# Kernel optimization log

Hardware: AMD Instinct MI355X
Metric: run time of the kernel (lower is better)

The kernel has to match this reference:

```python
import jax, jax.numpy as jnp
import numpy as np

DIM = 64
N_HOP = 2
N_MEM = 32
BATCH = 512
N_ENT = 200000
N_REL = 32
KGE_W = 0.01
L2_W = 1e-7
EPS = 1e-7  # BCE clamp for stability


def setup_inputs() -> dict:
    key = jax.random.key(0)
    ks = jax.random.split(key, 11)
    return {
        "items": jax.random.randint(ks[0], (BATCH,), 0, N_ENT),
        "labels": jax.random.randint(ks[1], (BATCH,), 0, 2),
        "memories_h": jax.random.randint(ks[2], (N_HOP, BATCH, N_MEM), 0, N_ENT),
        "memories_r": jax.random.randint(ks[3], (N_HOP, BATCH, N_MEM), 0, N_REL),
        "memories_t": jax.random.randint(ks[4], (N_HOP, BATCH, N_MEM), 0, N_ENT),
        "entity_emb": jax.random.normal(ks[5], (N_ENT, DIM), jnp.float32) * 0.1,
        "relation_emb": jax.random.normal(ks[6], (N_REL, DIM * DIM), jnp.float32) * 0.02,
        "gru_wih": jax.random.normal(ks[7], (3 * DIM, DIM), jnp.float32) * 0.1,
        "gru_whh": jax.random.normal(ks[8], (3 * DIM, DIM), jnp.float32) * 0.1,
        "gru_bih": jnp.zeros((3 * DIM,), jnp.float32),
        "gru_bhh": jnp.zeros((3 * DIM,), jnp.float32),
    }


def _gru_scan(x_seq, h0, wih, whh, bih, bhh):
    """PyTorch nn.GRU on a 2D input treats dim 0 as the sequence axis (unbatched).
    x_seq: [B, D] scanned over B; h0: [D]. Gate order: r, z, n."""
    def step(h, x):
        gi = wih @ x + bih          # [3D]
        gh = whh @ h + bhh          # [3D]
        ir, iz, inn = jnp.split(gi, 3)
        hr, hz, hn = jnp.split(gh, 3)
        r = jax.nn.sigmoid(ir + hr)
        z = jax.nn.sigmoid(iz + hz)
        n = jnp.tanh(inn + r * hn)
        h_new = (1.0 - z) * n + z * h
        return h_new, h_new
    h_final, ys = jax.lax.scan(step, h0, x_seq)
    return ys, h_final


def reference(items, labels, memories_h, memories_r, memories_t,
              entity_emb, relation_emb, gru_wih, gru_whh, gru_bih, gru_bhh):
    item_emb = entity_emb[items]                                # [B, D]
    h_emb = entity_emb[memories_h]                              # [H, B, M, D]
    t_emb = entity_emb[memories_t]                              # [H, B, M, D]
    r_flat = relation_emb[memories_r]                           # [H, B, M, D*D]
    r_emb = r_flat.reshape(N_HOP, BATCH, N_MEM, DIM, DIM)       # [H, B, M, D, D]

    h_state = jnp.zeros((DIM,), item_emb.dtype)
    o_sum = jnp.zeros_like(item_emb)
    for hop in range(N_HOP):
        Rh = jnp.einsum('bmij,bmj->bmi', r_emb[hop], h_emb[hop])   # [B, M, D]
        probs = jax.nn.softmax(jnp.einsum('bmi,bi->bm', Rh, item_emb), axis=1)
        o = jnp.einsum('bm,bmd->bd', probs, t_emb[hop])            # [B, D]
        # GRU recurrence over the batch axis (faithful to the 2D-input quirk)
        item_emb, h_state = _gru_scan(item_emb, h_state, gru_wih, gru_whh, gru_bih, gru_bhh)
        o_sum = o_sum + o  # using_all_hops=True -> sum of all hops

    scores = jax.nn.sigmoid(jnp.sum(item_emb * o_sum, axis=1))     # [B]

    # losses
    lbl = labels.astype(scores.dtype)
    s = jnp.clip(scores, EPS, 1.0 - EPS)
    base_loss = -jnp.mean(lbl * jnp.log(s) + (1.0 - lbl) * jnp.log1p(-s))

    hRt = jnp.einsum('hbmi,hbmij,hbmj->hbm', h_emb, r_emb, t_emb)  # [H, B, M]
    kge_loss = -KGE_W * jnp.sum(jnp.mean(jax.nn.sigmoid(hRt), axis=(1, 2)))

    l2_loss = L2_W * (jnp.sum(h_emb * h_emb) + jnp.sum(t_emb * t_emb) + jnp.sum(r_flat * r_flat))

    loss = base_loss + kge_loss + l2_loss
    return scores, base_loss, kge_loss, l2_loss, loss
```

## Files before the change

kernel.cpp:

```cpp
#include <hip/hip_runtime.h>

#define DIM   64
#define G3    192
#define NB    512
#define NM    32
#define NRELS 32
#define CH    32
#define NCH   (NB/CH)
#define KGE_W 0.01f
#define L2_W  1e-7f
#define EPSC  1e-7f


__device__ inline float bcast(float v, int srclane) {
    return __int_as_float(__builtin_amdgcn_readlane(__float_as_int(v), srclane));
}

__device__ inline float sigmoidf_(float x) { return 1.0f / (1.0f + __expf(-x)); }
__device__ inline float tanhf_(float x)    { return 1.0f - 2.0f / (1.0f + __expf(2.0f * x)); }

__device__ inline float wave_sum(float v) {
#pragma unroll
    for (int off = 32; off > 0; off >>= 1) v += __shfl_xor(v, off, 64);
    return v;
}
__device__ inline float wave_max(float v) {
#pragma unroll
    for (int off = 32; off > 0; off >>= 1) v = fmaxf(v, __shfl_xor(v, off, 64));
    return v;
}


#define FOR32(F) F(0)F(1)F(2)F(3)F(4)F(5)F(6)F(7)F(8)F(9)F(10)F(11)F(12)F(13)F(14)F(15) \
                 F(16)F(17)F(18)F(19)F(20)F(21)F(22)F(23)F(24)F(25)F(26)F(27)F(28)F(29)F(30)F(31)
#define FOR16A(F) F(0)F(1)F(2)F(3)F(4)F(5)F(6)F(7)F(8)F(9)F(10)F(11)F(12)F(13)F(14)F(15)
#define FOR16B(F) F(16)F(17)F(18)F(19)F(20)F(21)F(22)F(23)F(24)F(25)F(26)F(27)F(28)F(29)F(30)F(31)

#define F16U(x) ((unsigned)__builtin_bit_cast(unsigned short, (_Float16)(x)))


__device__ __forceinline__ void gru_scan_staged(float (*gibuf)[CH * G3],
                                                const float* __restrict__ GI,
                                                const float* __restrict__ whh,
                                                const float* __restrict__ bhh,
                                                const float* __restrict__ h0,
                                                float* __restrict__ ys,
                                                float* __restrict__ hfin_out)
{
    const int tid  = threadIdx.x;
    const int lane = tid & 63;
    const int wave = tid >> 6;

    if (wave != 0) {
        const int sid = tid - 64;
        const float4* src = (const float4*)GI;
        float4* dst = (float4*)gibuf[0];
#pragma unroll
        for (int j = 0; j < 8; ++j) dst[sid + j * 192] = src[sid + j * 192];
    }
    __syncthreads();

    if (wave == 0) {
        const float* wrp = whh + (0 * DIM + lane) * DIM;
        const float* wzp = whh + (1 * DIM + lane) * DIM;
        const float* wnp = whh + (2 * DIM + lane) * DIM;

#define DWP(j) unsigned uwr##j, uwz##j, uwn##j;
        FOR32(DWP)
#undef DWP
#define LWP(j) uwr##j = F16U(wrp[(j)]) | (F16U(wrp[(j)+32]) << 16); \
               uwz##j = F16U(wzp[(j)]) | (F16U(wzp[(j)+32]) << 16); \
               uwn##j = F16U(wnp[(j)]) | (F16U(wnp[(j)+32]) << 16);
        FOR32(LWP)
#undef LWP

        const float br = bhh[lane], bz = bhh[DIM + lane], bn = bhh[2 * DIM + lane];
        float h = h0 ? h0[lane] : 0.0f;

        for (int c = 0; c < NCH; ++c) {
            const float* buf = gibuf[c & 1];
            for (int tl = 0; tl < CH; ++tl) {
                const float* gi = buf + tl * G3;
                float c0 = gi[lane], c1 = gi[DIM + lane], c2 = gi[2 * DIM + lane];

                float A = h, B = h;
                asm("v_permlane32_swap_b32 %0, %1" : "+v"(A), "+v"(B));
                unsigned packed = __builtin_bit_cast(unsigned,
                                     __builtin_amdgcn_cvt_pkrtz(A, B));

#define RL(j) unsigned hp##j = (unsigned)__builtin_amdgcn_readlane((int)packed, j);
                FOR32(RL)
#undef RL

                float ar0 = br, ar1 = 0.f, az0 = bz, az1 = 0.f, an0 = bn, an1 = 0.f;
#define SJ0(j) { asm("v_dot2_f32_f16 %0, %1, %2, %0" : "+v"(ar0) : "v"(uwr##j), "s"(hp##j)); \
                 asm("v_dot2_f32_f16 %0, %1, %2, %0" : "+v"(az0) : "v"(uwz##j), "s"(hp##j)); \
                 asm("v_dot2_f32_f16 %0, %1, %2, %0" : "+v"(an0) : "v"(uwn##j), "s"(hp##j)); }
                FOR16A(SJ0)
#undef SJ0
#define SJ1(j) { asm("v_dot2_f32_f16 %0, %1, %2, %0" : "+v"(ar1) : "v"(uwr##j), "s"(hp##j)); \
                 asm("v_dot2_f32_f16 %0, %1, %2, %0" : "+v"(az1) : "v"(uwz##j), "s"(hp##j)); \
                 asm("v_dot2_f32_f16 %0, %1, %2, %0" : "+v"(an1) : "v"(uwn##j), "s"(hp##j)); }
                FOR16B(SJ1)
#undef SJ1

                float ghr = ar0 + ar1;
                float ghz = az0 + az1;
                float ghn = an0 + an1;

                float r = sigmoidf_(c0 + ghr);
                float z = sigmoidf_(c1 + ghz);
                float n = tanhf_(c2 + r * ghn);
                h = n + z * (h - n);

                ys[(c * CH + tl) * DIM + lane] = h;
            }
            __syncthreads();
        }
        if (hfin_out) hfin_out[lane] = h;
    } else {
        const int sid = tid - 64;
        for (int c = 0; c < NCH; ++c) {
            if (c + 1 < NCH) {
                const float4* src = (const float4*)(GI + (size_t)(c + 1) * CH * G3);
                float4* dst = (float4*)gibuf[(c + 1) & 1];
#pragma unroll
                for (int j = 0; j < 8; ++j) dst[sid + j * 192] = src[sid + j * 192];
            }
            __syncthreads();
        }
    }
}


__global__ __launch_bounds__(64) void gi_kernel(const float* __restrict__ xsrc,
                                                const int* __restrict__ idx,
                                                const float* __restrict__ wih,
                                                const float* __restrict__ bih,
                                                const float* __restrict__ Rel,
                                                float* __restrict__ GI,
                                                float* __restrict__ relnorm)
{
    const int blk = blockIdx.x, lane = threadIdx.x;
    if (blk >= NB) {
        const int r = blk - NB;
        const float* R = Rel + r * DIM * DIM;
        float a = 0.0f;
#pragma unroll 4
        for (int i = 0; i < DIM; ++i) { float v = R[i * DIM + lane]; a = fmaf(v, v, a); }
        a = wave_sum(a);
        if (lane == 0) relnorm[r] = a;
        return;
    }
    const int b = blk;
    float xv = idx ? xsrc[idx[b] * DIM + lane] : xsrc[b * DIM + lane];
    float a0 = bih[lane], a1 = bih[DIM + lane], a2 = bih[2 * DIM + lane];
    const float* w0 = wih + (0 * DIM + lane) * DIM;
    const float* w1 = wih + (1 * DIM + lane) * DIM;
    const float* w2 = wih + (2 * DIM + lane) * DIM;
#pragma unroll 4
    for (int k = 0; k < DIM; ++k) {
        float xk = bcast(xv, k);
        a0 = fmaf(w0[k], xk, a0);
        a1 = fmaf(w1[k], xk, a1);
        a2 = fmaf(w2[k], xk, a2);
    }
    float* gp = GI + b * G3;
    gp[lane] = a0; gp[DIM + lane] = a1; gp[2 * DIM + lane] = a2;
}


__global__ __launch_bounds__(256, 1) void fused0(const float* __restrict__ E,
                                              const float* __restrict__ Rel,
                                              const int* __restrict__ items,
                                              const int* __restrict__ mh,
                                              const int* __restrict__ mr,
                                              const int* __restrict__ mt,
                                              const float* __restrict__ GI,
                                              const float* __restrict__ whh,
                                              const float* __restrict__ bhh,
                                              const float* __restrict__ relnorm,
                                              float* __restrict__ ys0,
                                              float* __restrict__ hfin,
                                              float* __restrict__ o0,
                                              float* __restrict__ kge_part,
                                              float* __restrict__ l2_part)
{
    __shared__ __align__(16) float gibuf[2][CH * G3];
    __shared__ float logits[NM], probs[NM], opart[4][DIM], wred[4][4];

    if (blockIdx.x == 0) {
        gru_scan_staged(gibuf, GI, whh, bhh, nullptr, ys0, hfin);
        return;
    }

    const int b = blockIdx.x - 1;
    const int tid = threadIdx.x, lane = tid & 63, wave = tid >> 6;

    float iv = E[items[b] * DIM + lane];
    float kge0 = 0.0f, kge1 = 0.0f, l2acc = 0.0f, r2acc = 0.0f;

    for (int mm = 0; mm < 8; ++mm) {
        const int m = wave * 8 + mm;
        const int base = b * NM + m;
        const int hidx = mh[base], ridx = mr[base], tidx = mt[base];
        float hv = E[hidx * DIM + lane];
        float tv = E[tidx * DIM + lane];
        l2acc = fmaf(hv, hv, l2acc);
        l2acc = fmaf(tv, tv, l2acc);
        r2acc += relnorm[ridx];
        const float* R = Rel + ridx * DIM * DIM;
        float accA = 0.0f, accK = 0.0f;
#pragma unroll 4
        for (int i = 0; i < DIM; ++i) {
            float rv = R[i * DIM + lane];
            accA = fmaf(bcast(iv, i), rv, accA);
            accK = fmaf(bcast(hv, i), rv, accK);
        }
        float la = wave_sum(accA * hv);
        float lk = wave_sum(accK * tv);
        if (lane == 0) logits[m] = la;
        kge0 += sigmoidf_(lk);
    }
    for (int mm = 0; mm < 8; ++mm) {
        const int m = wave * 8 + mm;
        const int base = NB * NM + b * NM + m;
        const int hidx = mh[base], ridx = mr[base], tidx = mt[base];
        float hv = E[hidx * DIM + lane];
        float tv = E[tidx * DIM + lane];
        l2acc = fmaf(hv, hv, l2acc);
        l2acc = fmaf(tv, tv, l2acc);
        r2acc += relnorm[ridx];
        const float* R = Rel + ridx * DIM * DIM;
        float accK = 0.0f;
#pragma unroll 4
        for (int i = 0; i < DIM; ++i)
            accK = fmaf(bcast(hv, i), R[i * DIM + lane], accK);
        kge1 += sigmoidf_(wave_sum(accK * tv));
    }
    __syncthreads();

    if (wave == 0) {
        float v = (lane < NM) ? logits[lane] : -1e30f;
        float mx = wave_max(v);
        float e = (lane < NM) ? __expf(v - mx) : 0.0f;
        float ssum = wave_sum(e);
        if (lane < NM) probs[lane] = e / ssum;
    }
    __syncthreads();

    float od = 0.0f;
    for (int mm = 0; mm < 8; ++mm) {
        const int m = wave * 8 + mm;
        const int tidx = mt[b * NM + m];
        od = fmaf(probs[m], E[tidx * DIM + lane], od);
    }
    opart[wave][lane] = od;
    float l2tot = wave_sum(l2acc);
    if (lane == 0) { wred[wave][0] = kge0; wred[wave][1] = kge1; wred[wave][2] = l2tot + r2acc; }
    __syncthreads();
    if (wave == 0)
        o0[b * DIM + lane] = opart[0][lane] + opart[1][lane] + opart[2][lane] + opart[3][lane];
    if (tid == 0) {
        kge_part[b * 2 + 0] = wred[0][0] + wred[1][0] + wred[2][0] + wred[3][0];
        kge_part[b * 2 + 1] = wred[0][1] + wred[1][1] + wred[2][1] + wred[3][1];
        l2_part[b]          = wred[0][2] + wred[1][2] + wred[2][2] + wred[3][2];
    }
}


__global__ __launch_bounds__(256, 1) void fused1(const float* __restrict__ E,
                                              const float* __restrict__ Rel,
                                              const int* __restrict__ mh,
                                              const int* __restrict__ mr,
                                              const int* __restrict__ mt,
                                              const float* __restrict__ GI,
                                              const float* __restrict__ whh,
                                              const float* __restrict__ bhh,
                                              const float* __restrict__ hfin,
                                              const float* __restrict__ ys0,
                                              float* __restrict__ ys1,
                                              const float* __restrict__ o0,
                                              float* __restrict__ osum)
{
    __shared__ __align__(16) float gibuf[2][CH * G3];
    __shared__ float logits[NM], probs[NM], opart[4][DIM];

    if (blockIdx.x == 0) {
        gru_scan_staged(gibuf, GI, whh, bhh, hfin, ys1, nullptr);
        return;
    }

    const int b = blockIdx.x - 1;
    const int tid = threadIdx.x, lane = tid & 63, wave = tid >> 6;

    float iv = ys0[b * DIM + lane];

    for (int mm = 0; mm < 8; ++mm) {
        const int m = wave * 8 + mm;
        const int base = NB * NM + b * NM + m;
        const int hidx = mh[base], ridx = mr[base];
        float hv = E[hidx * DIM + lane];
        const float* R = Rel + ridx * DIM * DIM;
        float accA = 0.0f;
#pragma unroll 4
        for (int i = 0; i < DIM; ++i)
            accA = fmaf(bcast(iv, i), R[i * DIM + lane], accA);
        float la = wave_sum(accA * hv);
        if (lane == 0) logits[m] = la;
    }
    __syncthreads();
    if (wave == 0) {
        float v = (lane < NM) ? logits[lane] : -1e30f;
        float mx = wave_max(v);
        float e = (lane < NM) ? __expf(v - mx) : 0.0f;
        float ssum = wave_sum(e);
        if (lane < NM) probs[lane] = e / ssum;
    }
    __syncthreads();
    float od = 0.0f;
    for (int mm = 0; mm < 8; ++mm) {
        const int m = wave * 8 + mm;
        const int tidx = mt[NB * NM + b * NM + m];
        od = fmaf(probs[m], E[tidx * DIM + lane], od);
    }
    opart[wave][lane] = od;
    __syncthreads();
    if (wave == 0)
        osum[b * DIM + lane] = o0[b * DIM + lane] +
            opart[0][lane] + opart[1][lane] + opart[2][lane] + opart[3][lane];
}


__global__ __launch_bounds__(512) void finalize(const float* __restrict__ ys1,
                                                const float* __restrict__ osum,
                                                const int* __restrict__ labels,
                                                const float* __restrict__ kge_part,
                                                const float* __restrict__ l2_part,
                                                float* __restrict__ out)
{
    __shared__ float red[512];
    const int tid = threadIdx.x;

    float dot = 0.0f;
    const float* a = ys1 + tid * DIM;
    const float* c = osum + tid * DIM;
#pragma unroll 8
    for (int k = 0; k < DIM; ++k) dot = fmaf(a[k], c[k], dot);
    float score = sigmoidf_(dot);
    out[tid] = score;

    float s = fminf(fmaxf(score, EPSC), 1.0f - EPSC);
    float term = labels[tid] ? logf(s) : log1pf(-s);

    float bsum, ksum, lsum;
    {
        red[tid] = term; __syncthreads();
#pragma unroll
        for (int st = 256; st > 0; st >>= 1) { if (tid < st) red[tid] += red[tid + st]; __syncthreads(); }
        bsum = red[0]; __syncthreads();
    }
    {
        red[tid] = kge_part[2 * tid] + kge_part[2 * tid + 1]; __syncthreads();
#pragma unroll
        for (int st = 256; st > 0; st >>= 1) { if (tid < st) red[tid] += red[tid + st]; __syncthreads(); }
        ksum = red[0]; __syncthreads();
    }
    {
        red[tid] = l2_part[tid]; __syncthreads();
#pragma unroll
        for (int st = 256; st > 0; st >>= 1) { if (tid < st) red[tid] += red[tid + st]; __syncthreads(); }
        lsum = red[0];
    }

    if (tid == 0) {
        float base = -bsum / (float)NB;
        float kge  = -KGE_W * ksum / (float)(NB * NM);
        float l2   = L2_W * lsum;
        out[NB + 0] = base;
        out[NB + 1] = kge;
        out[NB + 2] = l2;
        out[NB + 3] = base + kge + l2;
    }
}


extern "C" void kernel_launch(void* const* d_in, const int* in_sizes, int n_in,
                              void* d_out, int out_size, void* d_ws, size_t ws_size,
                              hipStream_t stream) {
    const int*   items  = (const int*)d_in[0];
    const int*   labels = (const int*)d_in[1];
    const int*   mh     = (const int*)d_in[2];
    const int*   mr     = (const int*)d_in[3];
    const int*   mt     = (const int*)d_in[4];
    const float* E      = (const float*)d_in[5];
    const float* Rel    = (const float*)d_in[6];
    const float* wih    = (const float*)d_in[7];
    const float* whh    = (const float*)d_in[8];
    const float* bih    = (const float*)d_in[9];
    const float* bhh    = (const float*)d_in[10];
    float* out = (float*)d_out;
    float* ws  = (float*)d_ws;

    float* GI0     = ws;
    float* GI1     = GI0 + 98304;
    float* ys0     = GI1 + 98304;
    float* ys1     = ys0 + 32768;
    float* hfin    = ys1 + 32768;
    float* o0      = hfin + 64;
    float* osum    = o0 + 32768;
    float* relnorm = osum + 32768;
    float* kge_p   = relnorm + 32;
    float* l2_p    = kge_p + 1024;

    gi_kernel<<<NB + NRELS, 64, 0, stream>>>(E, items, wih, bih, Rel, GI0, relnorm);
    fused0<<<NB + 1, 256, 0, stream>>>(E, Rel, items, mh, mr, mt, GI0, whh, bhh,
                                       relnorm, ys0, hfin, o0, kge_p, l2_p);
    gi_kernel<<<NB, 64, 0, stream>>>(ys0, nullptr, wih, bih, Rel, GI1, relnorm);
    fused1<<<NB + 1, 256, 0, stream>>>(E, Rel, mh, mr, mt, GI1, whh, bhh, hfin,
                                       ys0, ys1, o0, osum);
    finalize<<<1, 512, 0, stream>>>(ys1, osum, labels, kge_p, l2_p, out);
}
```

Before: 452.4 us.

## Fuse hop-1 GRU input projection into hop-0 scan block and split dot chains

The second gi_kernel launch is removed. The helper waves in the GRU scan block now compute the hop-1 input projection (wih·ys0 + bih) in fp16 dot2, one chunk behind the sequential recurrence, and write it to GI1. The recurrence itself splits each gate's dot-product chain into four accumulators and computes r,z before n, to shorten dependency latency. Risks: fp16 rounding on the wih projection, and extra register pressure and work on the helper waves that share the serial scan's CU.

```diff
diff --git a/kernel.cpp b/kernel.cpp
--- a/kernel.cpp
+++ b/kernel.cpp
@@ -33,10 +33,31 @@
 
 #define FOR32(F) F(0)F(1)F(2)F(3)F(4)F(5)F(6)F(7)F(8)F(9)F(10)F(11)F(12)F(13)F(14)F(15) \
                  F(16)F(17)F(18)F(19)F(20)F(21)F(22)F(23)F(24)F(25)F(26)F(27)F(28)F(29)F(30)F(31)
-#define FOR16A(F) F(0)F(1)F(2)F(3)F(4)F(5)F(6)F(7)F(8)F(9)F(10)F(11)F(12)F(13)F(14)F(15)
-#define FOR16B(F) F(16)F(17)F(18)F(19)F(20)F(21)F(22)F(23)F(24)F(25)F(26)F(27)F(28)F(29)F(30)F(31)
+#define FOR8_0(F) F(0)F(1)F(2)F(3)F(4)F(5)F(6)F(7)
+#define FOR8_1(F) F(8)F(9)F(10)F(11)F(12)F(13)F(14)F(15)
+#define FOR8_2(F) F(16)F(17)F(18)F(19)F(20)F(21)F(22)F(23)
+#define FOR8_3(F) F(24)F(25)F(26)F(27)F(28)F(29)F(30)F(31)
 
 #define F16U(x) ((unsigned)__builtin_bit_cast(unsigned short, (_Float16)(x)))
+
+#define DOT(acc, w, s) asm("v_dot2_f32_f16 %0, %1, %2, %0" : "+v"(acc) : "v"(w), "s"(s));
+
+#define DW(j)  unsigned uwr##j, uwz##j, uwn##j;
+#define LW(j)  uwr##j = F16U(wrp[(j)]) | (F16U(wrp[(j)+32]) << 16); \
+               uwz##j = F16U(wzp[(j)]) | (F16U(wzp[(j)+32]) << 16); \
+               uwn##j = F16U(wnp[(j)]) | (F16U(wnp[(j)+32]) << 16);
+#define RLD(j) unsigned hp##j = (unsigned)__builtin_amdgcn_readlane((int)pk, j);
+
+#define SRZ_A(j) { DOT(pr0, uwr##j, hp##j) DOT(pz0, uwz##j, hp##j) }
+#define SRZ_B(j) { DOT(pr1, uwr##j, hp##j) DOT(pz1, uwz##j, hp##j) }
+#define SRZ_C(j) { DOT(pr2, uwr##j, hp##j) DOT(pz2, uwz##j, hp##j) }
+#define SRZ_D(j) { DOT(pr3, uwr##j, hp##j) DOT(pz3, uwz##j, hp##j) }
+#define SN_A(j)  { DOT(pn0, uwn##j, hp##j) }
+#define SN_B(j)  { DOT(pn1, uwn##j, hp##j) }
+#define SN_C(j)  { DOT(pn2, uwn##j, hp##j) }
+#define SN_D(j)  { DOT(pn3, uwn##j, hp##j) }
+#define DO_RZ FOR8_0(SRZ_A) FOR8_1(SRZ_B) FOR8_2(SRZ_C) FOR8_3(SRZ_D)
+#define DO_N  FOR8_0(SN_A)  FOR8_1(SN_B)  FOR8_2(SN_C)  FOR8_3(SN_D)
 
 
 __device__ __forceinline__ void gru_scan_staged(float (*gibuf)[CH * G3],
@@ -45,7 +66,10 @@
                                                 const float* __restrict__ bhh,
                                                 const float* __restrict__ h0,
                                                 float* __restrict__ ys,
-                                                float* __restrict__ hfin_out)
+                                                float* __restrict__ hfin_out,
+                                                const float* __restrict__ wih,
+                                                const float* __restrict__ bih,
+                                                float* __restrict__ gi1out)
 {
     const int tid  = threadIdx.x;
     const int lane = tid & 63;
@@ -64,16 +88,8 @@
         const float* wrp = whh + (0 * DIM + lane) * DIM;
         const float* wzp = whh + (1 * DIM + lane) * DIM;
         const float* wnp = whh + (2 * DIM + lane) * DIM;
-
-#define DWP(j) unsigned uwr##j, uwz##j, uwn##j;
-        FOR32(DWP)
-#undef DWP
-#define LWP(j) uwr##j = F16U(wrp[(j)]) | (F16U(wrp[(j)+32]) << 16); \
-               uwz##j = F16U(wzp[(j)]) | (F16U(wzp[(j)+32]) << 16); \
-               uwn##j = F16U(wnp[(j)]) | (F16U(wnp[(j)+32]) << 16);
-        FOR32(LWP)
-#undef LWP
-
+        FOR32(DW)
+        FOR32(LW)
         const float br = bhh[lane], bz = bhh[DIM + lane], bn = bhh[2 * DIM + lane];
         float h = h0 ? h0[lane] : 0.0f;
 
@@ -83,33 +99,23 @@
                 const float* gi = buf + tl * G3;
                 float c0 = gi[lane], c1 = gi[DIM + lane], c2 = gi[2 * DIM + lane];
 
-                float A = h, B = h;
-                asm("v_permlane32_swap_b32 %0, %1" : "+v"(A), "+v"(B));
-                unsigned packed = __builtin_bit_cast(unsigned,
-                                     __builtin_amdgcn_cvt_pkrtz(A, B));
-
-#define RL(j) unsigned hp##j = (unsigned)__builtin_amdgcn_readlane((int)packed, j);
-                FOR32(RL)
-#undef RL
-
-                float ar0 = br, ar1 = 0.f, az0 = bz, az1 = 0.f, an0 = bn, an1 = 0.f;
-#define SJ0(j) { asm("v_dot2_f32_f16 %0, %1, %2, %0" : "+v"(ar0) : "v"(uwr##j), "s"(hp##j)); \
-                 asm("v_dot2_f32_f16 %0, %1, %2, %0" : "+v"(az0) : "v"(uwz##j), "s"(hp##j)); \
-                 asm("v_dot2_f32_f16 %0, %1, %2, %0" : "+v"(an0) : "v"(uwn##j), "s"(hp##j)); }
-                FOR16A(SJ0)
-#undef SJ0
-#define SJ1(j) { asm("v_dot2_f32_f16 %0, %1, %2, %0" : "+v"(ar1) : "v"(uwr##j), "s"(hp##j)); \
-                 asm("v_dot2_f32_f16 %0, %1, %2, %0" : "+v"(az1) : "v"(uwz##j), "s"(hp##j)); \
-                 asm("v_dot2_f32_f16 %0, %1, %2, %0" : "+v"(an1) : "v"(uwn##j), "s"(hp##j)); }
-                FOR16B(SJ1)
-#undef SJ1
-
-                float ghr = ar0 + ar1;
-                float ghz = az0 + az1;
-                float ghn = an0 + an1;
-
+                float A_ = h, B_ = h;
+                asm("v_permlane32_swap_b32 %0, %1" : "+v"(A_), "+v"(B_));
+                unsigned pk = __builtin_bit_cast(unsigned,
+                                  __builtin_amdgcn_cvt_pkrtz(A_, B_));
+                FOR32(RLD)
+
+                float pr0 = br, pr1 = 0.f, pr2 = 0.f, pr3 = 0.f;
+                float pz0 = bz, pz1 = 0.f, pz2 = 0.f, pz3 = 0.f;
+                DO_RZ
+                float ghr = (pr0 + pr1) + (pr2 + pr3);
+                float ghz = (pz0 + pz1) + (pz2 + pz3);
                 float r = sigmoidf_(c0 + ghr);
                 float z = sigmoidf_(c1 + ghz);
+
+                float pn0 = bn, pn1 = 0.f, pn2 = 0.f, pn3 = 0.f;
+                DO_N
+                float ghn = (pn0 + pn1) + (pn2 + pn3);
                 float n = tanhf_(c2 + r * ghn);
                 h = n + z * (h - n);
 
@@ -120,6 +126,38 @@
         if (hfin_out) hfin_out[lane] = h;
     } else {
         const int sid = tid - 64;
+
+        const float* wrp = gi1out ? (wih + (0 * DIM + lane) * DIM) : whh;
+        const float* wzp = gi1out ? (wih + (1 * DIM + lane) * DIM) : whh;
+        const float* wnp = gi1out ? (wih + (2 * DIM + lane) * DIM) : whh;
+        FOR32(DW)
+        float br = 0.f, bz = 0.f, bn = 0.f;
+        if (gi1out) {
+            FOR32(LW)
+            br = bih[lane]; bz = bih[DIM + lane]; bn = bih[2 * DIM + lane];
+        }
+
+        auto gi1_chunk = [&](int cc) {
+            for (int t = wave - 1; t < CH; t += 3) {
+                const int gt = cc * CH + t;
+                float xv = ys[gt * DIM + lane];
+                float A_ = xv, B_ = xv;
+                asm("v_permlane32_swap_b32 %0, %1" : "+v"(A_), "+v"(B_));
+                unsigned pk = __builtin_bit_cast(unsigned,
+                                  __builtin_amdgcn_cvt_pkrtz(A_, B_));
+                FOR32(RLD)
+                float pr0 = br, pr1 = 0.f, pr2 = 0.f, pr3 = 0.f;
+                float pz0 = bz, pz1 = 0.f, pz2 = 0.f, pz3 = 0.f;
+                DO_RZ
+                float pn0 = bn, pn1 = 0.f, pn2 = 0.f, pn3 = 0.f;
+                DO_N
+                float* gp = gi1out + gt * G3;
+                gp[lane]           = (pr0 + pr1) + (pr2 + pr3);
+                gp[DIM + lane]     = (pz0 + pz1) + (pz2 + pz3);
+                gp[2 * DIM + lane] = (pn0 + pn1) + (pn2 + pn3);
+            }
+        };
+
         for (int c = 0; c < NCH; ++c) {
             if (c + 1 < NCH) {
                 const float4* src = (const float4*)(GI + (size_t)(c + 1) * CH * G3);
@@ -127,8 +165,10 @@
 #pragma unroll
                 for (int j = 0; j < 8; ++j) dst[sid + j * 192] = src[sid + j * 192];
             }
+            if (gi1out && c >= 1) gi1_chunk(c - 1);
             __syncthreads();
         }
+        if (gi1out) gi1_chunk(NCH - 1);
     }
 }
 
@@ -179,9 +219,12 @@
                                               const float* __restrict__ GI,
                                               const float* __restrict__ whh,
                                               const float* __restrict__ bhh,
+                                              const float* __restrict__ wih,
+                                              const float* __restrict__ bih,
                                               const float* __restrict__ relnorm,
                                               float* __restrict__ ys0,
                                               float* __restrict__ hfin,
+                                              float* __restrict__ GI1,
                                               float* __restrict__ o0,
                                               float* __restrict__ kge_part,
                                               float* __restrict__ l2_part)
@@ -190,7 +233,7 @@
     __shared__ float logits[NM], probs[NM], opart[4][DIM], wred[4][4];
 
     if (blockIdx.x == 0) {
-        gru_scan_staged(gibuf, GI, whh, bhh, nullptr, ys0, hfin);
+        gru_scan_staged(gibuf, GI, whh, bhh, nullptr, ys0, hfin, wih, bih, GI1);
         return;
     }
 
@@ -287,7 +330,7 @@
     __shared__ float logits[NM], probs[NM], opart[4][DIM];
 
     if (blockIdx.x == 0) {
-        gru_scan_staged(gibuf, GI, whh, bhh, hfin, ys1, nullptr);
+        gru_scan_staged(gibuf, GI, whh, bhh, hfin, ys1, nullptr, nullptr, nullptr, nullptr);
         return;
     }
 
@@ -415,8 +458,7 @@
 
     gi_kernel<<<NB + NRELS, 64, 0, stream>>>(E, items, wih, bih, Rel, GI0, relnorm);
     fused0<<<NB + 1, 256, 0, stream>>>(E, Rel, items, mh, mr, mt, GI0, whh, bhh,
-                                       relnorm, ys0, hfin, o0, kge_p, l2_p);
-    gi_kernel<<<NB, 64, 0, stream>>>(ys0, nullptr, wih, bih, Rel, GI1, relnorm);
+                                       wih, bih, relnorm, ys0, hfin, GI1, o0, kge_p, l2_p);
     fused1<<<NB + 1, 256, 0, stream>>>(E, Rel, mh, mr, mt, GI1, whh, bhh, hfin,
                                        ys0, ys1, o0, osum);
     finalize<<<1, 512, 0, stream>>>(ys1, osum, labels, kge_p, l2_p, out);
```

New measurement: 466.1 us. +3.0%, slower.
